# Performance work log

Measured on AMD Instinct MI355X. Metric: run time of the kernel, lower is better.

Reference implementation:

```python
import jax, jax.numpy as jnp
import numpy as np

B, D = 8192, 4096  # batch, dim


def setup_inputs() -> dict:
    key = jax.random.key(0)
    k1, k2, k3, k4 = jax.random.split(key, 4)
    y_true = jax.random.normal(k1, (B, D), dtype=jnp.float32)
    y_pred = jax.random.normal(k2, (B, D), dtype=jnp.float32)
    param = jax.random.normal(k3, (1,), dtype=jnp.float32)
    n = jax.random.randint(k4, (B,), 1, D + 1)  # valid lengths in [1, D]
    return {"y_true": y_true, "y_pred": y_pred, "param": param, "n": n}


def reference(y_true, y_pred, param, n):
    # AR(1) Mahalanobis loss. Precision P = I + coef*(superdiag + subdiag),
    # coef = -rho/(1+rho^2), rho = 2*sigmoid(param)-1. diag(diff @ P @ diff.T)
    # is computed directly as sum(diff * (P applied row-wise)), never
    # materializing P (D x D) or the batch x batch product.
    diff = y_true - y_pred                                   # [B, D]
    mask = jnp.arange(diff.shape[-1]) < n[:, None]           # filter_by_n
    diff = diff * mask
    rho = 2.0 * jax.nn.sigmoid(param[0]) - 1.0               # expit_m1
    coef = -rho / (1.0 + rho * rho)
    # tridiagonal matvec: (P d)_j = d_j + coef*(d_{j-1} + d_{j+1})
    neighbors = (jnp.pad(diff[:, 1:], ((0, 0), (0, 1)))
                 + jnp.pad(diff[:, :-1], ((0, 0), (1, 0))))  # [B, D]
    quad = jnp.sum(diff * (diff + coef * neighbors), axis=-1)  # [B]
    return jnp.mean(quad / n)
```

## Files before the change

kernel.cpp:

```cpp
#include <hip/hip_runtime.h>
#include <math.h>

#define B_ROWS 8192
#define D_DIM  4096

__global__ void mahal_init_kernel(double* __restrict__ acc) {
    if (threadIdx.x == 0 && blockIdx.x == 0) *acc = 0.0;
}

__global__ __launch_bounds__(256) void mahal_main_kernel(
    const float* __restrict__ y_true,
    const float* __restrict__ y_pred,
    const float* __restrict__ param,
    const int*   __restrict__ n,
    double*      __restrict__ acc)
{
    const int row = blockIdx.x;
    const int tid = threadIdx.x;
    const int ni  = n[row];

    const float* yt = y_true + (size_t)row * D_DIM;
    const float* yp = y_pred + (size_t)row * D_DIM;

    float sum_sq  = 0.f;
    float sum_adj = 0.f;

    #pragma unroll
    for (int it = 0; it < D_DIM / (256 * 4); ++it) {
        const int j = it * (256 * 4) + tid * 4;
        const float4 t = *reinterpret_cast<const float4*>(yt + j);
        const float4 p = *reinterpret_cast<const float4*>(yp + j);
        const float d0 = (j + 0 < ni) ? (t.x - p.x) : 0.f;
        const float d1 = (j + 1 < ni) ? (t.y - p.y) : 0.f;
        const float d2 = (j + 2 < ni) ? (t.z - p.z) : 0.f;
        const float d3 = (j + 3 < ni) ? (t.w - p.w) : 0.f;
        const float d4 = (j + 4 < ni) ? (yt[j + 4] - yp[j + 4]) : 0.f;

        sum_sq  += d0 * d0 + d1 * d1 + d2 * d2 + d3 * d3;
        sum_adj += d0 * d1 + d1 * d2 + d2 * d3 + d3 * d4;
    }

    #pragma unroll
    for (int off = 32; off > 0; off >>= 1) {
        sum_sq  += __shfl_down(sum_sq,  off, 64);
        sum_adj += __shfl_down(sum_adj, off, 64);
    }

    __shared__ float s_sq[4];
    __shared__ float s_adj[4];
    const int wave = tid >> 6;
    if ((tid & 63) == 0) { s_sq[wave] = sum_sq; s_adj[wave] = sum_adj; }
    __syncthreads();

    if (tid == 0) {
        const float tot_sq  = s_sq[0] + s_sq[1] + s_sq[2] + s_sq[3];
        const float tot_adj = s_adj[0] + s_adj[1] + s_adj[2] + s_adj[3];
        const float x    = param[0];
        const float rho  = 2.0f * (1.0f / (1.0f + expf(-x))) - 1.0f;
        const float coef = -rho / (1.0f + rho * rho);
        const double quad = (double)tot_sq + 2.0 * (double)coef * (double)tot_adj;
        atomicAdd(acc, quad / ((double)ni * (double)B_ROWS));
    }
}

__global__ void mahal_final_kernel(const double* __restrict__ acc,
                                   float* __restrict__ out) {
    if (threadIdx.x == 0 && blockIdx.x == 0) *out = (float)(*acc);
}

extern "C" void kernel_launch(void* const* d_in, const int* in_sizes, int n_in,
                              void* d_out, int out_size, void* d_ws, size_t ws_size,
                              hipStream_t stream) {
    const float* y_true = (const float*)d_in[0];
    const float* y_pred = (const float*)d_in[1];
    const float* param  = (const float*)d_in[2];
    const int*   n      = (const int*)d_in[3];
    float* out = (float*)d_out;
    double* acc = (double*)d_ws;

    mahal_init_kernel<<<1, 64, 0, stream>>>(acc);
    mahal_main_kernel<<<B_ROWS, 256, 0, stream>>>(y_true, y_pred, param, n, acc);
    mahal_final_kernel<<<1, 64, 0, stream>>>(acc, out);
}
```

Baseline: 303.2 us.

## Skip loads beyond valid length, share neighbors via LDS, replace atomics with two-stage reduce

Each thread now loads its float4 chunks only when the chunk start lies inside the row's valid length n, so masked tail data is not read from global memory. The extra scalar neighbor load is replaced by exchanging the first element of each chunk through shared memory. The per-row double atomicAdd and the init kernel are replaced by per-row float2 partials, which a single-block final kernel reduces in double. This adds a __syncthreads and some shared memory traffic, and the reduction order changes slightly.

After: 249.4 us. 1.22x faster.

```diff
diff --git a/kernel.cpp b/kernel.cpp
--- a/kernel.cpp
+++ b/kernel.cpp
@@ -4,40 +4,54 @@
 #define B_ROWS 8192
 #define D_DIM  4096
 
-__global__ void mahal_init_kernel(double* __restrict__ acc) {
-    if (threadIdx.x == 0 && blockIdx.x == 0) *acc = 0.0;
-}
-
 __global__ __launch_bounds__(256) void mahal_main_kernel(
     const float* __restrict__ y_true,
     const float* __restrict__ y_pred,
-    const float* __restrict__ param,
     const int*   __restrict__ n,
-    double*      __restrict__ acc)
+    float2*      __restrict__ partial)
 {
     const int row = blockIdx.x;
     const int tid = threadIdx.x;
     const int ni  = n[row];
 
-    const float* yt = y_true + (size_t)row * D_DIM;
-    const float* yp = y_pred + (size_t)row * D_DIM;
+    const float4* yt4 = reinterpret_cast<const float4*>(y_true + (size_t)row * D_DIM);
+    const float4* yp4 = reinterpret_cast<const float4*>(y_pred + (size_t)row * D_DIM);
 
-    float sum_sq  = 0.f;
-    float sum_adj = 0.f;
+    float4 t[4], p[4];
+    #pragma unroll
+    for (int it = 0; it < 4; ++it) {
+        const int j = (it << 10) + (tid << 2);
+        t[it] = make_float4(0.f, 0.f, 0.f, 0.f);
+        p[it] = make_float4(0.f, 0.f, 0.f, 0.f);
+        if (j < ni) {
+            t[it] = yt4[it * 256 + tid];
+            p[it] = yp4[it * 256 + tid];
+        }
+    }
 
+    __shared__ float s0[4][257];
+    float d[4][4];
     #pragma unroll
-    for (int it = 0; it < D_DIM / (256 * 4); ++it) {
-        const int j = it * (256 * 4) + tid * 4;
-        const float4 t = *reinterpret_cast<const float4*>(yt + j);
-        const float4 p = *reinterpret_cast<const float4*>(yp + j);
-        const float d0 = (j + 0 < ni) ? (t.x - p.x) : 0.f;
-        const float d1 = (j + 1 < ni) ? (t.y - p.y) : 0.f;
-        const float d2 = (j + 2 < ni) ? (t.z - p.z) : 0.f;
-        const float d3 = (j + 3 < ni) ? (t.w - p.w) : 0.f;
-        const float d4 = (j + 4 < ni) ? (yt[j + 4] - yp[j + 4]) : 0.f;
+    for (int it = 0; it < 4; ++it) {
+        const int j = (it << 10) + (tid << 2);
+        d[it][0] = (j + 0 < ni) ? (t[it].x - p[it].x) : 0.f;
+        d[it][1] = (j + 1 < ni) ? (t[it].y - p[it].y) : 0.f;
+        d[it][2] = (j + 2 < ni) ? (t[it].z - p[it].z) : 0.f;
+        d[it][3] = (j + 3 < ni) ? (t[it].w - p[it].w) : 0.f;
+        s0[it][tid] = d[it][0];
+    }
+    __syncthreads();
 
-        sum_sq  += d0 * d0 + d1 * d1 + d2 * d2 + d3 * d3;
-        sum_adj += d0 * d1 + d1 * d2 + d2 * d3 + d3 * d4;
+    float sum_sq = 0.f, sum_adj = 0.f;
+    #pragma unroll
+    for (int it = 0; it < 4; ++it) {
+        float nb;
+        if (tid < 255) nb = s0[it][tid + 1];
+        else           nb = (it < 3) ? s0[it + 1][0] : 0.f;
+        sum_sq  += d[it][0] * d[it][0] + d[it][1] * d[it][1]
+                 + d[it][2] * d[it][2] + d[it][3] * d[it][3];
+        sum_adj += d[it][0] * d[it][1] + d[it][1] * d[it][2]
+                 + d[it][2] * d[it][3] + d[it][3] * nb;
     }
 
     #pragma unroll
@@ -46,26 +60,50 @@
         sum_adj += __shfl_down(sum_adj, off, 64);
     }
 
-    __shared__ float s_sq[4];
-    __shared__ float s_adj[4];
+    __shared__ float r_sq[4], r_adj[4];
     const int wave = tid >> 6;
-    if ((tid & 63) == 0) { s_sq[wave] = sum_sq; s_adj[wave] = sum_adj; }
+    if ((tid & 63) == 0) { r_sq[wave] = sum_sq; r_adj[wave] = sum_adj; }
     __syncthreads();
 
     if (tid == 0) {
-        const float tot_sq  = s_sq[0] + s_sq[1] + s_sq[2] + s_sq[3];
-        const float tot_adj = s_adj[0] + s_adj[1] + s_adj[2] + s_adj[3];
+        const float inv_n = 1.0f / (float)ni;
+        const float ssq   = r_sq[0] + r_sq[1] + r_sq[2] + r_sq[3];
+        const float sadj  = r_adj[0] + r_adj[1] + r_adj[2] + r_adj[3];
+        partial[row] = make_float2(ssq * inv_n, sadj * inv_n);
+    }
+}
+
+__global__ __launch_bounds__(256) void mahal_final_kernel(
+    const float2* __restrict__ partial,
+    const float*  __restrict__ param,
+    float*        __restrict__ out)
+{
+    const int tid = threadIdx.x;
+    const float4* p4 = reinterpret_cast<const float4*>(partial);
+    double s1 = 0.0, s2 = 0.0;
+    #pragma unroll
+    for (int it = 0; it < 16; ++it) {
+        const float4 v = p4[it * 256 + tid];
+        s1 += (double)v.x + (double)v.z;
+        s2 += (double)v.y + (double)v.w;
+    }
+    #pragma unroll
+    for (int off = 32; off > 0; off >>= 1) {
+        s1 += __shfl_down(s1, off, 64);
+        s2 += __shfl_down(s2, off, 64);
+    }
+    __shared__ double w1[4], w2[4];
+    const int wave = tid >> 6;
+    if ((tid & 63) == 0) { w1[wave] = s1; w2[wave] = s2; }
+    __syncthreads();
+    if (tid == 0) {
+        const double S1 = w1[0] + w1[1] + w1[2] + w1[3];
+        const double S2 = w2[0] + w2[1] + w2[2] + w2[3];
         const float x    = param[0];
         const float rho  = 2.0f * (1.0f / (1.0f + expf(-x))) - 1.0f;
         const float coef = -rho / (1.0f + rho * rho);
-        const double quad = (double)tot_sq + 2.0 * (double)coef * (double)tot_adj;
-        atomicAdd(acc, quad / ((double)ni * (double)B_ROWS));
+        *out = (float)((S1 + 2.0 * (double)coef * S2) / (double)B_ROWS);
     }
-}
-
-__global__ void mahal_final_kernel(const double* __restrict__ acc,
-                                   float* __restrict__ out) {
-    if (threadIdx.x == 0 && blockIdx.x == 0) *out = (float)(*acc);
 }
 
 extern "C" void kernel_launch(void* const* d_in, const int* in_sizes, int n_in,
@@ -76,9 +114,8 @@
     const float* param  = (const float*)d_in[2];
     const int*   n      = (const int*)d_in[3];
     float* out = (float*)d_out;
-    double* acc = (double*)d_ws;
+    float2* partial = (float2*)d_ws;
 
-    mahal_init_kernel<<<1, 64, 0, stream>>>(acc);
-    mahal_main_kernel<<<B_ROWS, 256, 0, stream>>>(y_true, y_pred, param, n, acc);
-    mahal_final_kernel<<<1, 64, 0, stream>>>(acc, out);
+    mahal_main_kernel<<<B_ROWS, 256, 0, stream>>>(y_true, y_pred, n, partial);
+    mahal_final_kernel<<<1, 256, 0, stream>>>(partial, param, out);
 }
```

## Skip loads past valid length, shuffle neighbors, replace atomic with partial reduction

Applied to the files above, without the earlier changes.

Loads of y_true/y_pred are predicated on the valid length n, so masked tail elements are never read from memory. Each wave now covers a contiguous 1024-element span, and the right neighbor comes from a lane shuffle instead of an extra scalar load. The double atomicAdd and init kernel are replaced by per-row float partials reduced by a single-block final kernel. The risk is slightly different float rounding, from the per-row float division and from combining the two sums into one before reduction.

Measured after the change: 248.8 us. 17.9% less time.

```diff
diff --git a/kernel.cpp b/kernel.cpp
--- a/kernel.cpp
+++ b/kernel.cpp
@@ -4,68 +4,98 @@
 #define B_ROWS 8192
 #define D_DIM  4096
 
-__global__ void mahal_init_kernel(double* __restrict__ acc) {
-    if (threadIdx.x == 0 && blockIdx.x == 0) *acc = 0.0;
-}
-
 __global__ __launch_bounds__(256) void mahal_main_kernel(
     const float* __restrict__ y_true,
     const float* __restrict__ y_pred,
     const float* __restrict__ param,
     const int*   __restrict__ n,
-    double*      __restrict__ acc)
+    float*       __restrict__ partial)
 {
-    const int row = blockIdx.x;
-    const int tid = threadIdx.x;
-    const int ni  = n[row];
+    const int row  = blockIdx.x;
+    const int tid  = threadIdx.x;
+    const int lane = tid & 63;
+    const int w    = tid >> 6;
+    const int ni   = n[row];
 
     const float* yt = y_true + (size_t)row * D_DIM;
     const float* yp = y_pred + (size_t)row * D_DIM;
+    const int base = (w << 10) + (lane << 2);
 
-    float sum_sq  = 0.f;
-    float sum_adj = 0.f;
+    float4 t[4], p[4];
+    #pragma unroll
+    for (int q = 0; q < 4; ++q) {
+        const int j = base + (q << 8);
+        t[q] = make_float4(0.f, 0.f, 0.f, 0.f);
+        p[q] = make_float4(0.f, 0.f, 0.f, 0.f);
+        if (j < ni) {
+            t[q] = *reinterpret_cast<const float4*>(yt + j);
+            p[q] = *reinterpret_cast<const float4*>(yp + j);
+        }
+    }
+    float bnd = 0.f;
+    if (lane == 63) {
+        const int e = (w + 1) << 10;
+        if (e < ni) bnd = yt[e] - yp[e];
+    }
+
+    float d[4][4];
+    #pragma unroll
+    for (int q = 0; q < 4; ++q) {
+        const int j = base + (q << 8);
+        d[q][0] = (j + 0 < ni) ? (t[q].x - p[q].x) : 0.f;
+        d[q][1] = (j + 1 < ni) ? (t[q].y - p[q].y) : 0.f;
+        d[q][2] = (j + 2 < ni) ? (t[q].z - p[q].z) : 0.f;
+        d[q][3] = (j + 3 < ni) ? (t[q].w - p[q].w) : 0.f;
+    }
+
+    float ssq = 0.f, sadj = 0.f;
+    #pragma unroll
+    for (int q = 0; q < 4; ++q) {
+        float nb = __shfl_down(d[q][0], 1, 64);
+        const float bq = (q < 3) ? __shfl(d[q + 1 < 4 ? q + 1 : 3][0], 0, 64) : bnd;
+        if (lane == 63) nb = bq;
+        ssq  += d[q][0] * d[q][0] + d[q][1] * d[q][1]
+              + d[q][2] * d[q][2] + d[q][3] * d[q][3];
+        sadj += d[q][0] * d[q][1] + d[q][1] * d[q][2]
+              + d[q][2] * d[q][3] + d[q][3] * nb;
+    }
+
+    const float x    = param[0];
+    const float rho  = 2.0f * (1.0f / (1.0f + expf(-x))) - 1.0f;
+    const float coef = -rho / (1.0f + rho * rho);
+    float quad = ssq + 2.0f * coef * sadj;
 
     #pragma unroll
-    for (int it = 0; it < D_DIM / (256 * 4); ++it) {
-        const int j = it * (256 * 4) + tid * 4;
-        const float4 t = *reinterpret_cast<const float4*>(yt + j);
-        const float4 p = *reinterpret_cast<const float4*>(yp + j);
-        const float d0 = (j + 0 < ni) ? (t.x - p.x) : 0.f;
-        const float d1 = (j + 1 < ni) ? (t.y - p.y) : 0.f;
-        const float d2 = (j + 2 < ni) ? (t.z - p.z) : 0.f;
-        const float d3 = (j + 3 < ni) ? (t.w - p.w) : 0.f;
-        const float d4 = (j + 4 < ni) ? (yt[j + 4] - yp[j + 4]) : 0.f;
+    for (int off = 32; off > 0; off >>= 1)
+        quad += __shfl_down(quad, off, 64);
 
-        sum_sq  += d0 * d0 + d1 * d1 + d2 * d2 + d3 * d3;
-        sum_adj += d0 * d1 + d1 * d2 + d2 * d3 + d3 * d4;
-    }
-
-    #pragma unroll
-    for (int off = 32; off > 0; off >>= 1) {
-        sum_sq  += __shfl_down(sum_sq,  off, 64);
-        sum_adj += __shfl_down(sum_adj, off, 64);
-    }
-
-    __shared__ float s_sq[4];
-    __shared__ float s_adj[4];
-    const int wave = tid >> 6;
-    if ((tid & 63) == 0) { s_sq[wave] = sum_sq; s_adj[wave] = sum_adj; }
+    __shared__ float r[4];
+    if (lane == 0) r[w] = quad;
     __syncthreads();
-
-    if (tid == 0) {
-        const float tot_sq  = s_sq[0] + s_sq[1] + s_sq[2] + s_sq[3];
-        const float tot_adj = s_adj[0] + s_adj[1] + s_adj[2] + s_adj[3];
-        const float x    = param[0];
-        const float rho  = 2.0f * (1.0f / (1.0f + expf(-x))) - 1.0f;
-        const float coef = -rho / (1.0f + rho * rho);
-        const double quad = (double)tot_sq + 2.0 * (double)coef * (double)tot_adj;
-        atomicAdd(acc, quad / ((double)ni * (double)B_ROWS));
-    }
+    if (tid == 0)
+        partial[row] = (r[0] + r[1] + r[2] + r[3]) / (float)ni;
 }
 
-__global__ void mahal_final_kernel(const double* __restrict__ acc,
-                                   float* __restrict__ out) {
-    if (threadIdx.x == 0 && blockIdx.x == 0) *out = (float)(*acc);
+__global__ __launch_bounds__(256) void mahal_final_kernel(
+    const float* __restrict__ partial,
+    float*       __restrict__ out)
+{
+    const int tid = threadIdx.x;
+    const float4* p4 = reinterpret_cast<const float4*>(partial);
+    double s = 0.0;
+    #pragma unroll
+    for (int it = 0; it < 8; ++it) {
+        const float4 v = p4[it * 256 + tid];
+        s += (double)v.x + (double)v.y + (double)v.z + (double)v.w;
+    }
+    #pragma unroll
+    for (int off = 32; off > 0; off >>= 1)
+        s += __shfl_down(s, off, 64);
+    __shared__ double wsum[4];
+    if ((tid & 63) == 0) wsum[tid >> 6] = s;
+    __syncthreads();
+    if (tid == 0)
+        *out = (float)((wsum[0] + wsum[1] + wsum[2] + wsum[3]) / (double)B_ROWS);
 }
 
 extern "C" void kernel_launch(void* const* d_in, const int* in_sizes, int n_in,
@@ -76,9 +106,8 @@
     const float* param  = (const float*)d_in[2];
     const int*   n      = (const int*)d_in[3];
     float* out = (float*)d_out;
-    double* acc = (double*)d_ws;
+    float* partial = (float*)d_ws;
 
-    mahal_init_kernel<<<1, 64, 0, stream>>>(acc);
-    mahal_main_kernel<<<B_ROWS, 256, 0, stream>>>(y_true, y_pred, param, n, acc);
-    mahal_final_kernel<<<1, 64, 0, stream>>>(acc, out);
+    mahal_main_kernel<<<B_ROWS, 256, 0, stream>>>(y_true, y_pred, param, n, partial);
+    mahal_final_kernel<<<1, 256, 0, stream>>>(partial, out);
 }
```
